# Kernel optimization log

Measured on AMD Instinct MI355X. Metric: run time of the kernel, lower is better.

## Reference

```python
import jax, jax.numpy as jnp
import numpy as np
from itertools import chain, combinations

OBS_DIM = 4096
LAT = 64
NG = 4
GS = OBS_DIM // NG  # 1024 features per group (round-robin i % NG == g)
B = 8192


def _powerset_mask(n):
    subsets = list(chain.from_iterable(combinations(range(n), r) for r in range(1, n + 1)))
    m = np.zeros((len(subsets), n), np.float32)
    for i, s in enumerate(subsets):
        m[i, list(s)] = 1.0
    return jnp.asarray(m)


SUBSET_MASK = _powerset_mask(NG)  # [S, G], S = 2^G - 1 = 15
GROUP_IDX = jnp.asarray(np.stack([np.arange(g, OBS_DIM, NG) for g in range(NG)]), dtype=jnp.int32)  # [G, GS]


def setup_inputs() -> dict:
    key = jax.random.key(0)
    ks = jax.random.split(key, 11)
    s = 0.05
    H = 2 * LAT  # encoder hidden / output width
    return {
        "X": jax.random.normal(ks[0], (B, OBS_DIM), jnp.float32),
        "eps": jax.random.normal(ks[1], (B, LAT), jnp.float32),
        "subset_idx": jax.random.randint(ks[2], (B,), 0, SUBSET_MASK.shape[0], dtype=jnp.int32),
        "enc_w1": jax.random.normal(ks[3], (NG, GS, H), jnp.float32) * s,
        "enc_b1": jnp.zeros((NG, H), jnp.float32),
        "enc_w2": jax.random.normal(ks[4], (NG, H, H), jnp.float32) * s,
        "enc_b2": jnp.zeros((NG, H), jnp.float32),
        "dec_w1": jax.random.normal(ks[5], (NG, LAT, LAT), jnp.float32) * s,
        "dec_b1": jnp.zeros((NG, LAT), jnp.float32),
        "dec_w2": jax.random.normal(ks[6], (NG, LAT, GS), jnp.float32) * s,
        "dec_b2": jnp.zeros((NG, GS), jnp.float32),
    }


def reference(X, eps, subset_idx, enc_w1, enc_b1, enc_w2, enc_b2, dec_w1, dec_b1, dec_w2, dec_b2):
    # ---- encode: per-group gather + tiny MLP (depth=2) ----
    Xg = X[:, GROUP_IDX]  # [B, G, GS] gather of group columns
    h = jax.nn.relu(jnp.einsum('bgi,gih->bgh', Xg, enc_w1) + enc_b1[None])  # [B, G, 2L]
    ml = jnp.einsum('bgh,gho->bgo', h, enc_w2) + enc_b2[None]               # [B, G, 2L]
    means, logvars = jnp.split(ml, 2, axis=-1)  # each [B, G, L]
    means = jnp.transpose(means, (0, 2, 1))     # [B, L, G] (tf stacks groups on axis=2)
    logvars = jnp.transpose(logvars, (0, 2, 1))

    # ---- mopoe: PoE over every non-empty subset of groups ----
    taus = jnp.exp(-logvars)                                   # [B, L, G]
    tau = jnp.einsum('blg,sg->bls', taus, SUBSET_MASK) + 1.0   # [B, L, S] (normalize_outp=True adds 1)
    m_means = jnp.einsum('blg,sg->bls', taus * means, SUBSET_MASK) / tau
    m_logvars = -jnp.log(tau)                                  # log(1/tau)

    # ---- reparameterize: pick one random subset per batch row ----
    sel = subset_idx[:, None, None].astype(jnp.int32)          # [B, 1, 1]
    smean = jnp.take_along_axis(m_means, sel, axis=-1)[..., 0]    # [B, L]
    slogv = jnp.take_along_axis(m_logvars, sel, axis=-1)[..., 0]  # [B, L]
    z = smean + eps * jnp.exp(0.5 * slogv)                     # [B, L]

    # ---- decode: per-group tiny MLP, scatter back to obs_dim ----
    hd = jax.nn.relu(jnp.einsum('bl,glm->bgm', z, dec_w1) + dec_b1[None])  # [B, G, L]
    outg = jnp.einsum('bgm,gmo->bgo', hd, dec_w2) + dec_b2[None]            # [B, G, GS]
    recon = jnp.zeros((X.shape[0], OBS_DIM), X.dtype).at[:, GROUP_IDX.reshape(-1)].set(
        outg.reshape(X.shape[0], -1))
    return recon
```

## Files before the change

### kernel.cpp

```cpp
#include <hip/hip_runtime.h>
#include <hip/hip_bf16.h>
#include <math.h>

#define B_TOT 8192
#define OBS   4096
#define NG    4
#define GSZ   1024
#define LATD  64
#define HDIM  128

#define RS   136
#define PLA  2184
#define PSH  648

typedef __attribute__((ext_vector_type(8))) short   short8_t;
typedef __attribute__((ext_vector_type(8))) unsigned short ushort8_t;
typedef __attribute__((ext_vector_type(4))) float   float4_t;

__constant__ int kMask[15] = {1,2,4,8, 3,5,9,6,10,12, 7,11,13,14, 15};

static __device__ __forceinline__ unsigned short f2b(float x) {
  __hip_bfloat16 b = __float2bfloat16(x);
  return *reinterpret_cast<unsigned short*>(&b);
}
static __device__ __forceinline__ unsigned int pack2(float lo, float hi) {
  return (unsigned int)f2b(lo) | ((unsigned int)f2b(hi) << 16);
}

#define N1 524288
#define N2 65536
#define N3 16384
#define N4 262144
__global__ __launch_bounds__(256) void k_prep(const float* __restrict__ w1,
                                              const float* __restrict__ w2,
                                              const float* __restrict__ w3,
                                              const float* __restrict__ w4,
                                              unsigned short* __restrict__ W1p,
                                              unsigned short* __restrict__ W2p,
                                              unsigned short* __restrict__ W3p,
                                              unsigned short* __restrict__ W4p) {
  const int i = blockIdx.x * 256 + threadIdx.x;
  if (i < N1) {
    const int j = i & 7, oct = (i >> 3) & 3, l15 = (i >> 5) & 15;
    const int ni = (i >> 9) & 3, ks = (i >> 11) & 3, c = (i >> 13) & 7;
    const int h2 = (i >> 16) & 1, g = (i >> 17) & 3;
    const int k = c * 128 + (j & 3) * 32 + ks * 8 + oct * 2 + (j >> 2);
    const int h = h2 * 64 + ni * 16 + l15;
    W1p[i] = f2b(w1[g * 131072 + k * 128 + h]);
  } else if (i < N1 + N2) {
    const int idx = i - N1;
    const int j = idx & 7, oct = (idx >> 3) & 3, l15 = (idx >> 5) & 15;
    const int ni = (idx >> 9) & 3, ks = (idx >> 11) & 3;
    const int h2 = (idx >> 13) & 1, g = (idx >> 14) & 3;
    const int k = ks * 32 + oct * 8 + j;
    const int h = h2 * 64 + ni * 16 + l15;
    W2p[idx] = f2b(w2[g * 16384 + k * 128 + h]);
  } else if (i < N1 + N2 + N3) {
    const int idx = i - N1 - N2;
    const int j = idx & 7, oct = (idx >> 3) & 3, l15 = (idx >> 5) & 15;
    const int ni = (idx >> 9) & 1, ks = (idx >> 10) & 1;
    const int h2 = (idx >> 11) & 1, g = (idx >> 12) & 3;
    const int k = ks * 32 + oct * 8 + j;
    const int m = h2 * 32 + ni * 16 + l15;
    W3p[idx] = f2b(w3[g * 4096 + k * 64 + m]);
  } else if (i < N1 + N2 + N3 + N4) {
    const int idx = i - N1 - N2 - N3;
    const int j = idx & 7, oct = (idx >> 3) & 3, l15 = (idx >> 5) & 15;
    const int ni = (idx >> 9) & 1, ks = (idx >> 10) & 1;
    const int oh = (idx >> 11) & 1, ob = (idx >> 12) & 15, g = (idx >> 16) & 3;
    const int k = ks * 32 + oct * 8 + j;
    const int o = ob * 64 + oh * 32 + ni * 16 + l15;
    W4p[idx] = f2b(w4[g * 65536 + k * 1024 + o]);
  }
}

struct EncLds {
  union {
    unsigned short lA[2][4 * PLA];
    unsigned short hp[16 * PSH];
    float mls[16][516];
  } u;
  unsigned short zb[16][72];
};
__global__ __launch_bounds__(512, 4) void k_enc(const float* __restrict__ X,
                                                const unsigned short* __restrict__ W1p,
                                                const unsigned short* __restrict__ W2p,
                                                const unsigned short* __restrict__ W3p,
                                                const float* __restrict__ B1,
                                                const float* __restrict__ B2,
                                                const float* __restrict__ DB1,
                                                const float* __restrict__ eps,
                                                const int*   __restrict__ subset_idx,
                                                unsigned short* __restrict__ Hd) {
  __shared__ EncLds s;
  const int tid = threadIdx.x;
  const int w   = tid >> 6;
  const int l   = tid & 63;
  const int g   = w >> 1;
  const int h2  = w & 1;
  const int rb  = blockIdx.x * 16;
  const int l15 = l & 15;
  const int oct = l >> 4;
  const int lofs = (l15 * 4 + oct) * 8;

  const int srow = tid >> 5;
  const int seg  = tid & 31;
  const float* xb = X + (size_t)(rb + srow) * OBS + seg * 4;

  float4_t q0, q1, q2, q3;
  q0 = *(const float4_t*)(xb + 0);
  q1 = *(const float4_t*)(xb + 128);
  q2 = *(const float4_t*)(xb + 256);
  q3 = *(const float4_t*)(xb + 384);
  {
#pragma unroll
    for (int gg = 0; gg < 4; ++gg) {
      uint2 v;
      v.x = pack2(q0[gg], q1[gg]);
      v.y = pack2(q2[gg], q3[gg]);
      *(uint2*)&s.u.lA[0][gg * PLA + srow * RS + seg * 4] = v;
    }
  }

  float4_t acc[4];
#pragma unroll
  for (int j = 0; j < 4; ++j) acc[j] = (float4_t){0.f, 0.f, 0.f, 0.f};

  const unsigned short* bb1 = W1p + (g * 2 + h2) * 65536 + lofs;

  for (int c = 0; c < 8; ++c) {
    __syncthreads();
    const int cur = c & 1;
    if (c < 7) {
      const float* xn = xb + (c + 1) * 512;
      q0 = *(const float4_t*)(xn + 0);
      q1 = *(const float4_t*)(xn + 128);
      q2 = *(const float4_t*)(xn + 256);
      q3 = *(const float4_t*)(xn + 384);
    }
#pragma unroll
    for (int ks = 0; ks < 4; ++ks) {
      const short8_t af = *(const short8_t*)&s.u.lA[cur][g * PLA + l15 * RS + ks * 32 + oct * 8];
      short8_t bf[4];
#pragma unroll
      for (int ni = 0; ni < 4; ++ni)
        bf[ni] = *(const short8_t*)(bb1 + c * 8192 + ks * 2048 + ni * 512);
#pragma unroll
      for (int ni = 0; ni < 4; ++ni)
        acc[ni] = __builtin_amdgcn_mfma_f32_16x16x32_bf16(af, bf[ni], acc[ni], 0, 0, 0);
    }
    if (c < 7) {
#pragma unroll
      for (int gg = 0; gg < 4; ++gg) {
        uint2 v;
        v.x = pack2(q0[gg], q1[gg]);
        v.y = pack2(q2[gg], q3[gg]);
        *(uint2*)&s.u.lA[cur ^ 1][gg * PLA + srow * RS + seg * 4] = v;
      }
    }
  }
  __syncthreads();

#pragma unroll
  for (int ni = 0; ni < 4; ++ni) {
    const int hcol = h2 * 64 + ni * 16 + l15;
    const float b  = B1[g * 128 + hcol];
    const int plane = (hcol >> 5) * 4 + g;
    const int off   = hcol & 31;
#pragma unroll
    for (int j = 0; j < 4; ++j)
      s.u.hp[plane * PSH + (oct * 4 + j) * 40 + off] = f2b(fmaxf(acc[ni][j] + b, 0.0f));
  }
  __syncthreads();

#pragma unroll
  for (int j = 0; j < 4; ++j) acc[j] = (float4_t){0.f, 0.f, 0.f, 0.f};
  {
    const unsigned short* bb2 = W2p + (g * 2 + h2) * 8192 + lofs;
#pragma unroll
    for (int ks = 0; ks < 4; ++ks) {
      const short8_t af = *(const short8_t*)&s.u.hp[(ks * 4 + g) * PSH + l15 * 40 + oct * 8];
#pragma unroll
      for (int ni = 0; ni < 4; ++ni) {
        const short8_t bf = *(const short8_t*)(bb2 + ks * 2048 + ni * 512);
        acc[ni] = __builtin_amdgcn_mfma_f32_16x16x32_bf16(af, bf, acc[ni], 0, 0, 0);
      }
    }
  }
  __syncthreads();

#pragma unroll
  for (int ni = 0; ni < 4; ++ni) {
    const int col = g * 128 + h2 * 64 + ni * 16 + l15;
    const float b = B2[col];
#pragma unroll
    for (int j = 0; j < 4; ++j)
      s.u.mls[oct * 4 + j][col] = acc[ni][j] + b;
  }
  __syncthreads();

#pragma unroll
  for (int qq = 0; qq < 2; ++qq) {
    const int idx = qq * 512 + tid;
    const int r   = idx >> 6;
    const int ll  = idx & 63;
    const int m   = kMask[subset_idx[rb + r]];
    float tau = 1.0f, num = 0.0f;
#pragma unroll
    for (int gg = 0; gg < 4; ++gg) {
      if (m & (1 << gg)) {
        const float lv = s.u.mls[r][gg * 128 + 64 + ll];
        const float mu = s.u.mls[r][gg * 128 + ll];
        const float t  = expf(-lv);
        tau += t;
        num = fmaf(t, mu, num);
      }
    }
    const float zv = num / tau + eps[(size_t)(rb + r) * LATD + ll] * rsqrtf(tau);
    s.zb[r][ll] = f2b(zv);
  }
  __syncthreads();

  float4_t a3[2];
  a3[0] = (float4_t){0.f, 0.f, 0.f, 0.f};
  a3[1] = (float4_t){0.f, 0.f, 0.f, 0.f};
  {
    const unsigned short* bb3 = W3p + (g * 2 + h2) * 2048 + lofs;
#pragma unroll
    for (int ks = 0; ks < 2; ++ks) {
      const short8_t af = *(const short8_t*)&s.zb[l15][ks * 32 + oct * 8];
#pragma unroll
      for (int ni = 0; ni < 2; ++ni) {
        const short8_t bf = *(const short8_t*)(bb3 + ks * 1024 + ni * 512);
        a3[ni] = __builtin_amdgcn_mfma_f32_16x16x32_bf16(af, bf, a3[ni], 0, 0, 0);
      }
    }
  }
#pragma unroll
  for (int ni = 0; ni < 2; ++ni) {
    const int col = g * 64 + h2 * 32 + ni * 16 + l15;
    const float b = DB1[col];
#pragma unroll
    for (int j = 0; j < 4; ++j)
      Hd[(size_t)(rb + oct * 4 + j) * 256 + col] = f2b(fmaxf(a3[ni][j] + b, 0.0f));
  }
}

__global__ __launch_bounds__(512) void k_dec2(const unsigned short* __restrict__ Hd,
                                              const unsigned short* __restrict__ W4p,
                                              const float* __restrict__ Bb,
                                              float* __restrict__ Out) {
  __shared__ float obuf[32][264];

  const int tid = threadIdx.x;
  const int w   = tid >> 6;
  const int l   = tid & 63;
  const int g   = w >> 1;
  const int oh  = w & 1;
  const int r0  = blockIdx.x * 32;
  const int ob  = blockIdx.y * 64;
  const int l15 = l & 15;
  const int oct = l >> 4;
  const int lofs = (l15 * 4 + oct) * 8;

  float4_t acc[2][2];
#pragma unroll
  for (int i = 0; i < 2; ++i)
#pragma unroll
    for (int j = 0; j < 2; ++j) acc[i][j] = (float4_t){0.f, 0.f, 0.f, 0.f};

  const unsigned short* bb4 = W4p + ((g * 16 + blockIdx.y) * 2 + oh) * 2048 + lofs;

#pragma unroll
  for (int ks = 0; ks < 2; ++ks) {
    short8_t af[2], bf[2];
#pragma unroll
    for (int mi = 0; mi < 2; ++mi)
      af[mi] = *(const short8_t*)(Hd + (size_t)(r0 + mi * 16 + l15) * 256 +
                                  g * 64 + ks * 32 + oct * 8);
#pragma unroll
    for (int ni = 0; ni < 2; ++ni)
      bf[ni] = *(const short8_t*)(bb4 + ks * 1024 + ni * 512);
#pragma unroll
    for (int mi = 0; mi < 2; ++mi)
#pragma unroll
      for (int ni = 0; ni < 2; ++ni)
        acc[mi][ni] = __builtin_amdgcn_mfma_f32_16x16x32_bf16(af[mi], bf[ni], acc[mi][ni], 0, 0, 0);
  }

#pragma unroll
  for (int ni = 0; ni < 2; ++ni) {
    const int lo = oh * 32 + ni * 16 + l15;
    const float b = Bb[g * 1024 + ob + lo];
#pragma unroll
    for (int mi = 0; mi < 2; ++mi) {
      const int rloc = mi * 16 + oct * 4;
#pragma unroll
      for (int j = 0; j < 4; ++j)
        obuf[rloc + j][4 * lo + g] = acc[mi][ni][j] + b;
    }
  }
  __syncthreads();

#pragma unroll
  for (int i = 0; i < 4; ++i) {
    const int q = tid + i * 512;
    const int row = q >> 6, c4 = q & 63;
    const float4 v = *(const float4*)&obuf[row][c4 * 4];
    *(float4*)(Out + (size_t)(r0 + row) * OBS + 4 * ob + c4 * 4) = v;
  }
}

extern "C" void kernel_launch(void* const* d_in, const int* in_sizes, int n_in,
                              void* d_out, int out_size, void* d_ws, size_t ws_size,
                              hipStream_t stream) {
  const float* X          = (const float*)d_in[0];
  const float* eps        = (const float*)d_in[1];
  const int*   subset_idx = (const int*)  d_in[2];
  const float* enc_w1     = (const float*)d_in[3];
  const float* enc_b1     = (const float*)d_in[4];
  const float* enc_w2     = (const float*)d_in[5];
  const float* enc_b2     = (const float*)d_in[6];
  const float* dec_w1     = (const float*)d_in[7];
  const float* dec_b1     = (const float*)d_in[8];
  const float* dec_w2     = (const float*)d_in[9];
  const float* dec_b2     = (const float*)d_in[10];
  float* out = (float*)d_out;

  char* wsb = (char*)d_ws;
  unsigned short* Hd  = (unsigned short*)wsb;
  unsigned short* W1p = (unsigned short*)(wsb + (4u << 20));
  unsigned short* W2p = (unsigned short*)(wsb + (5u << 20));
  unsigned short* W3p = (unsigned short*)(wsb + (5u << 20) + (128u << 10));
  unsigned short* W4p = (unsigned short*)(wsb + (5u << 20) + (160u << 10));

  k_prep<<<3392, 256, 0, stream>>>(enc_w1, enc_w2, dec_w1, dec_w2,
                                   W1p, W2p, W3p, W4p);
  k_enc<<<512, 512, 0, stream>>>(X, W1p, W2p, W3p, enc_b1, enc_b2, dec_b1,
                                 eps, subset_idx, Hd);
  k_dec2<<<dim3(256, 16), 512, 0, stream>>>(Hd, W4p, dec_b2, out);
}
```

Baseline: 103.5 us.

## Split encoder into de-interleave pass, per-group first-layer GEMM, and fused second stage

Adds a separate kernel that converts X to bf16 and de-interleaves the round-robin groups into a contiguous workspace. The first encoder layer then runs as its own per-group GEMM over 32-row tiles, with each wave producing a 2x2 block of MFMA tiles. The second layer, PoE and the decoder's first layer move into a smaller fused kernel. Weight packing is reordered to match. This aims for better weight reuse and occupancy in the dominant GEMM, but adds an extra full pass over X (a 64MB bf16 write plus reread) and more kernel launches.

```diff
diff --git a/kernel.cpp b/kernel.cpp
--- a/kernel.cpp
+++ b/kernel.cpp
@@ -8,10 +8,6 @@
 #define GSZ   1024
 #define LATD  64
 #define HDIM  128
-
-#define RS   136
-#define PLA  2184
-#define PSH  648
 
 typedef __attribute__((ext_vector_type(8))) short   short8_t;
 typedef __attribute__((ext_vector_type(8))) unsigned short ushort8_t;
@@ -42,26 +38,24 @@
   const int i = blockIdx.x * 256 + threadIdx.x;
   if (i < N1) {
     const int j = i & 7, oct = (i >> 3) & 3, l15 = (i >> 5) & 15;
-    const int ni = (i >> 9) & 3, ks = (i >> 11) & 3, c = (i >> 13) & 7;
-    const int h2 = (i >> 16) & 1, g = (i >> 17) & 3;
-    const int k = c * 128 + (j & 3) * 32 + ks * 8 + oct * 2 + (j >> 2);
-    const int h = h2 * 64 + ni * 16 + l15;
+    const int ni = (i >> 9) & 1, ks = (i >> 10) & 31;
+    const int w = (i >> 15) & 3, g = (i >> 17) & 3;
+    const int k = ks * 32 + oct * 8 + j;
+    const int h = w * 32 + ni * 16 + l15;
     W1p[i] = f2b(w1[g * 131072 + k * 128 + h]);
   } else if (i < N1 + N2) {
     const int idx = i - N1;
     const int j = idx & 7, oct = (idx >> 3) & 3, l15 = (idx >> 5) & 15;
-    const int ni = (idx >> 9) & 3, ks = (idx >> 11) & 3;
-    const int h2 = (idx >> 13) & 1, g = (idx >> 14) & 3;
+    const int ni = (idx >> 9) & 7, ks = (idx >> 12) & 3, g = (idx >> 14) & 3;
     const int k = ks * 32 + oct * 8 + j;
-    const int h = h2 * 64 + ni * 16 + l15;
-    W2p[idx] = f2b(w2[g * 16384 + k * 128 + h]);
+    const int col = ni * 16 + l15;
+    W2p[idx] = f2b(w2[g * 16384 + k * 128 + col]);
   } else if (i < N1 + N2 + N3) {
     const int idx = i - N1 - N2;
     const int j = idx & 7, oct = (idx >> 3) & 3, l15 = (idx >> 5) & 15;
-    const int ni = (idx >> 9) & 1, ks = (idx >> 10) & 1;
-    const int h2 = (idx >> 11) & 1, g = (idx >> 12) & 3;
+    const int ni = (idx >> 9) & 3, ks = (idx >> 11) & 1, g = (idx >> 12) & 3;
     const int k = ks * 32 + oct * 8 + j;
-    const int m = h2 * 32 + ni * 16 + l15;
+    const int m = ni * 16 + l15;
     W3p[idx] = f2b(w3[g * 4096 + k * 64 + m]);
   } else if (i < N1 + N2 + N3 + N4) {
     const int idx = i - N1 - N2 - N3;
@@ -74,115 +68,142 @@
   }
 }
 
-struct EncLds {
-  union {
-    unsigned short lA[2][4 * PLA];
-    unsigned short hp[16 * PSH];
-    float mls[16][516];
-  } u;
-  unsigned short zb[16][72];
-};
-__global__ __launch_bounds__(512, 4) void k_enc(const float* __restrict__ X,
-                                                const unsigned short* __restrict__ W1p,
-                                                const unsigned short* __restrict__ W2p,
-                                                const unsigned short* __restrict__ W3p,
-                                                const float* __restrict__ B1,
-                                                const float* __restrict__ B2,
-                                                const float* __restrict__ DB1,
-                                                const float* __restrict__ eps,
-                                                const int*   __restrict__ subset_idx,
-                                                unsigned short* __restrict__ Hd) {
-  __shared__ EncLds s;
+__global__ __launch_bounds__(512) void k_prepx(const float* __restrict__ X,
+                                               unsigned short* __restrict__ Xt) {
+  const int t = threadIdx.x;
+  const int b = blockIdx.x * 2 + (t >> 8);
+  const int c = (t & 255) * 16;
+  const float* p = X + (size_t)b * OBS + c;
+  const float4_t f0 = *(const float4_t*)(p);
+  const float4_t f1 = *(const float4_t*)(p + 4);
+  const float4_t f2 = *(const float4_t*)(p + 8);
+  const float4_t f3 = *(const float4_t*)(p + 12);
+  const int k0 = c >> 2;
+  unsigned short* q = Xt + (size_t)b * OBS;
+#pragma unroll
+  for (int g = 0; g < 4; ++g) {
+    uint2 v;
+    v.x = pack2(f0[g], f1[g]);
+    v.y = pack2(f2[g], f3[g]);
+    *(uint2*)(q + g * GSZ + k0) = v;
+  }
+}
+
+#define ARS 1032
+__global__ __launch_bounds__(256, 2) void k_enc1(const unsigned short* __restrict__ Xt,
+                                                 const unsigned short* __restrict__ W1p,
+                                                 const float* __restrict__ B1,
+                                                 unsigned short* __restrict__ Hbf) {
+  __shared__ union {
+    unsigned short lA[32 * ARS];
+    unsigned short ob[32][136];
+  } s;
   const int tid = threadIdx.x;
   const int w   = tid >> 6;
   const int l   = tid & 63;
-  const int g   = w >> 1;
-  const int h2  = w & 1;
-  const int rb  = blockIdx.x * 16;
   const int l15 = l & 15;
   const int oct = l >> 4;
+  const int rb  = blockIdx.x * 32;
+  const int g   = blockIdx.y;
   const int lofs = (l15 * 4 + oct) * 8;
 
-  const int srow = tid >> 5;
-  const int seg  = tid & 31;
-  const float* xb = X + (size_t)(rb + srow) * OBS + seg * 4;
-
-  float4_t q0, q1, q2, q3;
-  q0 = *(const float4_t*)(xb + 0);
-  q1 = *(const float4_t*)(xb + 128);
-  q2 = *(const float4_t*)(xb + 256);
-  q3 = *(const float4_t*)(xb + 384);
-  {
-#pragma unroll
-    for (int gg = 0; gg < 4; ++gg) {
-      uint2 v;
-      v.x = pack2(q0[gg], q1[gg]);
-      v.y = pack2(q2[gg], q3[gg]);
-      *(uint2*)&s.u.lA[0][gg * PLA + srow * RS + seg * 4] = v;
-    }
-  }
-
-  float4_t acc[4];
-#pragma unroll
-  for (int j = 0; j < 4; ++j) acc[j] = (float4_t){0.f, 0.f, 0.f, 0.f};
-
-  const unsigned short* bb1 = W1p + (g * 2 + h2) * 65536 + lofs;
-
-  for (int c = 0; c < 8; ++c) {
-    __syncthreads();
-    const int cur = c & 1;
-    if (c < 7) {
-      const float* xn = xb + (c + 1) * 512;
-      q0 = *(const float4_t*)(xn + 0);
-      q1 = *(const float4_t*)(xn + 128);
-      q2 = *(const float4_t*)(xn + 256);
-      q3 = *(const float4_t*)(xn + 384);
-    }
+  {
+    const int row = tid >> 3, seg = tid & 7;
+    const unsigned short* src = Xt + (size_t)(rb + row) * OBS + g * GSZ + seg * 128;
+    unsigned short* dst = &s.lA[row * ARS + seg * 128];
+#pragma unroll
+    for (int i = 0; i < 16; ++i)
+      *(ushort8_t*)(dst + i * 8) = *(const ushort8_t*)(src + i * 8);
+  }
+  __syncthreads();
+
+  float4_t acc[2][2];
+#pragma unroll
+  for (int i = 0; i < 2; ++i)
+#pragma unroll
+    for (int j = 0; j < 2; ++j) acc[i][j] = (float4_t){0.f, 0.f, 0.f, 0.f};
+
+  const unsigned short* bb = W1p + (size_t)(g * 4 + w) * 32768 + lofs;
+
+#pragma unroll 4
+  for (int ks = 0; ks < 32; ++ks) {
+    short8_t af[2], bf[2];
+#pragma unroll
+    for (int mi = 0; mi < 2; ++mi)
+      af[mi] = *(const short8_t*)&s.lA[(mi * 16 + l15) * ARS + ks * 32 + oct * 8];
+#pragma unroll
+    for (int ni = 0; ni < 2; ++ni)
+      bf[ni] = *(const short8_t*)(bb + ks * 1024 + ni * 512);
+#pragma unroll
+    for (int mi = 0; mi < 2; ++mi)
+#pragma unroll
+      for (int ni = 0; ni < 2; ++ni)
+        acc[mi][ni] = __builtin_amdgcn_mfma_f32_16x16x32_bf16(af[mi], bf[ni], acc[mi][ni], 0, 0, 0);
+  }
+  __syncthreads();
+
+#pragma unroll
+  for (int ni = 0; ni < 2; ++ni) {
+    const int hcol = w * 32 + ni * 16 + l15;
+    const float b = B1[g * 128 + hcol];
+#pragma unroll
+    for (int mi = 0; mi < 2; ++mi)
+#pragma unroll
+      for (int j = 0; j < 4; ++j)
+        s.ob[mi * 16 + oct * 4 + j][hcol] = f2b(fmaxf(acc[mi][ni][j] + b, 0.0f));
+  }
+  __syncthreads();
+  {
+    const int row = tid >> 3, ch = tid & 7;
+    unsigned short* dst = Hbf + (size_t)(rb + row) * 512 + g * 128 + ch * 16;
+    *(ushort8_t*)(dst)     = *(const ushort8_t*)&s.ob[row][ch * 16];
+    *(ushort8_t*)(dst + 8) = *(const ushort8_t*)&s.ob[row][ch * 16 + 8];
+  }
+}
+
+__global__ __launch_bounds__(256, 4) void k_enc2(const unsigned short* __restrict__ Hbf,
+                                                 const unsigned short* __restrict__ W2p,
+                                                 const unsigned short* __restrict__ W3p,
+                                                 const float* __restrict__ B2,
+                                                 const float* __restrict__ DB1,
+                                                 const float* __restrict__ eps,
+                                                 const int*   __restrict__ subset_idx,
+                                                 unsigned short* __restrict__ Hd) {
+  __shared__ union {
+    unsigned short hs[16][520];
+    float mls[16][516];
+  } u;
+  __shared__ unsigned short zb[16][72];
+
+  const int tid = threadIdx.x;
+  const int g   = tid >> 6;
+  const int l   = tid & 63;
+  const int l15 = l & 15;
+  const int oct = l >> 4;
+  const int rb  = blockIdx.x * 16;
+  const int lofs = (l15 * 4 + oct) * 8;
+
+  {
+    const int row = tid >> 4, p = tid & 15;
+    const unsigned short* src = Hbf + (size_t)(rb + row) * 512;
+#pragma unroll
+    for (int i = 0; i < 4; ++i)
+      *(ushort8_t*)&u.hs[row][p * 8 + i * 128] =
+          *(const ushort8_t*)(src + p * 8 + i * 128);
+  }
+  __syncthreads();
+
+  float4_t acc[8];
+#pragma unroll
+  for (int j = 0; j < 8; ++j) acc[j] = (float4_t){0.f, 0.f, 0.f, 0.f};
+  {
+    const unsigned short* bb = W2p + (size_t)g * 16384 + lofs;
 #pragma unroll
     for (int ks = 0; ks < 4; ++ks) {
-      const short8_t af = *(const short8_t*)&s.u.lA[cur][g * PLA + l15 * RS + ks * 32 + oct * 8];
-      short8_t bf[4];
-#pragma unroll
-      for (int ni = 0; ni < 4; ++ni)
-        bf[ni] = *(const short8_t*)(bb1 + c * 8192 + ks * 2048 + ni * 512);
-#pragma unroll
-      for (int ni = 0; ni < 4; ++ni)
-        acc[ni] = __builtin_amdgcn_mfma_f32_16x16x32_bf16(af, bf[ni], acc[ni], 0, 0, 0);
-    }
-    if (c < 7) {
-#pragma unroll
-      for (int gg = 0; gg < 4; ++gg) {
-        uint2 v;
-        v.x = pack2(q0[gg], q1[gg]);
-        v.y = pack2(q2[gg], q3[gg]);
-        *(uint2*)&s.u.lA[cur ^ 1][gg * PLA + srow * RS + seg * 4] = v;
-      }
-    }
-  }
-  __syncthreads();
-
-#pragma unroll
-  for (int ni = 0; ni < 4; ++ni) {
-    const int hcol = h2 * 64 + ni * 16 + l15;
-    const float b  = B1[g * 128 + hcol];
-    const int plane = (hcol >> 5) * 4 + g;
-    const int off   = hcol & 31;
-#pragma unroll
-    for (int j = 0; j < 4; ++j)
-      s.u.hp[plane * PSH + (oct * 4 + j) * 40 + off] = f2b(fmaxf(acc[ni][j] + b, 0.0f));
-  }
-  __syncthreads();
-
-#pragma unroll
-  for (int j = 0; j < 4; ++j) acc[j] = (float4_t){0.f, 0.f, 0.f, 0.f};
-  {
-    const unsigned short* bb2 = W2p + (g * 2 + h2) * 8192 + lofs;
-#pragma unroll
-    for (int ks = 0; ks < 4; ++ks) {
-      const short8_t af = *(const short8_t*)&s.u.hp[(ks * 4 + g) * PSH + l15 * 40 + oct * 8];
-#pragma unroll
-      for (int ni = 0; ni < 4; ++ni) {
-        const short8_t bf = *(const short8_t*)(bb2 + ks * 2048 + ni * 512);
+      const short8_t af = *(const short8_t*)&u.hs[l15][g * 128 + ks * 32 + oct * 8];
+#pragma unroll
+      for (int ni = 0; ni < 8; ++ni) {
+        const short8_t bf = *(const short8_t*)(bb + ks * 4096 + ni * 512);
         acc[ni] = __builtin_amdgcn_mfma_f32_16x16x32_bf16(af, bf, acc[ni], 0, 0, 0);
       }
     }
@@ -190,18 +211,18 @@
   __syncthreads();
 
 #pragma unroll
-  for (int ni = 0; ni < 4; ++ni) {
-    const int col = g * 128 + h2 * 64 + ni * 16 + l15;
+  for (int ni = 0; ni < 8; ++ni) {
+    const int col = g * 128 + ni * 16 + l15;
     const float b = B2[col];
 #pragma unroll
     for (int j = 0; j < 4; ++j)
-      s.u.mls[oct * 4 + j][col] = acc[ni][j] + b;
-  }
-  __syncthreads();
-
-#pragma unroll
-  for (int qq = 0; qq < 2; ++qq) {
-    const int idx = qq * 512 + tid;
+      u.mls[oct * 4 + j][col] = acc[ni][j] + b;
+  }
+  __syncthreads();
+
+#pragma unroll
+  for (int qq = 0; qq < 4; ++qq) {
+    const int idx = qq * 256 + tid;
     const int r   = idx >> 6;
     const int ll  = idx & 63;
     const int m   = kMask[subset_idx[rb + r]];
@@ -209,36 +230,36 @@
 #pragma unroll
     for (int gg = 0; gg < 4; ++gg) {
       if (m & (1 << gg)) {
-        const float lv = s.u.mls[r][gg * 128 + 64 + ll];
-        const float mu = s.u.mls[r][gg * 128 + ll];
+        const float lv = u.mls[r][gg * 128 + 64 + ll];
+        const float mu = u.mls[r][gg * 128 + ll];
         const float t  = expf(-lv);
         tau += t;
         num = fmaf(t, mu, num);
       }
     }
     const float zv = num / tau + eps[(size_t)(rb + r) * LATD + ll] * rsqrtf(tau);
-    s.zb[r][ll] = f2b(zv);
-  }
-  __syncthreads();
-
-  float4_t a3[2];
-  a3[0] = (float4_t){0.f, 0.f, 0.f, 0.f};
-  a3[1] = (float4_t){0.f, 0.f, 0.f, 0.f};
-  {
-    const unsigned short* bb3 = W3p + (g * 2 + h2) * 2048 + lofs;
+    zb[r][ll] = f2b(zv);
+  }
+  __syncthreads();
+
+  float4_t a3[4];
+#pragma unroll
+  for (int j = 0; j < 4; ++j) a3[j] = (float4_t){0.f, 0.f, 0.f, 0.f};
+  {
+    const unsigned short* bb = W3p + (size_t)g * 4096 + lofs;
 #pragma unroll
     for (int ks = 0; ks < 2; ++ks) {
-      const short8_t af = *(const short8_t*)&s.zb[l15][ks * 32 + oct * 8];
-#pragma unroll
-      for (int ni = 0; ni < 2; ++ni) {
-        const short8_t bf = *(const short8_t*)(bb3 + ks * 1024 + ni * 512);
+      const short8_t af = *(const short8_t*)&zb[l15][ks * 32 + oct * 8];
+#pragma unroll
+      for (int ni = 0; ni < 4; ++ni) {
+        const short8_t bf = *(const short8_t*)(bb + ks * 2048 + ni * 512);
         a3[ni] = __builtin_amdgcn_mfma_f32_16x16x32_bf16(af, bf, a3[ni], 0, 0, 0);
       }
     }
   }
 #pragma unroll
-  for (int ni = 0; ni < 2; ++ni) {
-    const int col = g * 64 + h2 * 32 + ni * 16 + l15;
+  for (int ni = 0; ni < 4; ++ni) {
+    const int col = g * 64 + ni * 16 + l15;
     const float b = DB1[col];
 #pragma unroll
     for (int j = 0; j < 4; ++j)
@@ -328,15 +349,19 @@
   float* out = (float*)d_out;
 
   char* wsb = (char*)d_ws;
-  unsigned short* Hd  = (unsigned short*)wsb;
-  unsigned short* W1p = (unsigned short*)(wsb + (4u << 20));
-  unsigned short* W2p = (unsigned short*)(wsb + (5u << 20));
-  unsigned short* W3p = (unsigned short*)(wsb + (5u << 20) + (128u << 10));
-  unsigned short* W4p = (unsigned short*)(wsb + (5u << 20) + (160u << 10));
+  unsigned short* Xt  = (unsigned short*)wsb;
+  unsigned short* Hbf = (unsigned short*)(wsb + (64u << 20));
+  unsigned short* Hd  = (unsigned short*)(wsb + (72u << 20));
+  unsigned short* W1p = (unsigned short*)(wsb + (76u << 20));
+  unsigned short* W2p = (unsigned short*)(wsb + (77u << 20));
+  unsigned short* W3p = (unsigned short*)(wsb + (77u << 20) + (128u << 10));
+  unsigned short* W4p = (unsigned short*)(wsb + (77u << 20) + (160u << 10));
 
   k_prep<<<3392, 256, 0, stream>>>(enc_w1, enc_w2, dec_w1, dec_w2,
                                    W1p, W2p, W3p, W4p);
-  k_enc<<<512, 512, 0, stream>>>(X, W1p, W2p, W3p, enc_b1, enc_b2, dec_b1,
-                                 eps, subset_idx, Hd);
+  k_prepx<<<4096, 512, 0, stream>>>(X, Xt);
+  k_enc1<<<dim3(256, 4), 256, 0, stream>>>(Xt, W1p, enc_b1, Hbf);
+  k_enc2<<<512, 256, 0, stream>>>(Hbf, W2p, W3p, enc_b2, dec_b1,
+                                  eps, subset_idx, Hd);
   k_dec2<<<dim3(256, 16), 512, 0, stream>>>(Hd, W4p, dec_b2, out);
 }
```

Result: slower. 145.7 us (+40.7%).
